# Kernel tuning notes

Hardware: AMD Instinct MI355X
Metric: run time of the kernel (lower is better)

## Reference

```python
import jax, jax.numpy as jnp
import numpy as np

NEG_SLOPE = 0.01
EPS = 1e-5


def leaky_relu(x):
    return jnp.where(x >= 0, x, NEG_SLOPE * x)


def graph_conv(x, W, src, dst, edge_weight, num_nodes):
    # DGL GraphConv, norm='both', bias=False: D_out^{-1/2} A_w D_in^{-1/2} X W
    ones = jnp.ones_like(edge_weight)
    deg_out = jnp.maximum(jax.ops.segment_sum(ones, src, num_segments=num_nodes), 1.0)
    deg_in = jnp.maximum(jax.ops.segment_sum(ones, dst, num_segments=num_nodes), 1.0)
    h = x @ W
    h = h * jax.lax.rsqrt(deg_out)[:, None]
    agg = jax.ops.segment_sum(h[src] * edge_weight[:, None], dst, num_segments=num_nodes)
    return agg * jax.lax.rsqrt(deg_in)[:, None]


def graph_norm(x, alpha, gamma, beta, batch_size):
    # GraphNorm: per-graph, per-channel mean/var; graphs are equal-sized -> reshape
    n = x.shape[0] // batch_size
    xg = x.reshape(batch_size, n, x.shape[1])
    mean = xg.mean(axis=1, keepdims=True)
    sub = xg - alpha * mean
    var = (sub * sub).mean(axis=1, keepdims=True)
    out = gamma * sub * jax.lax.rsqrt(var + EPS) + beta
    return out.reshape(x.shape)


def instance_norm(x):
    # InstanceNorm1d (affine=False) on 2D input: per-row normalization over features
    mean = x.mean(axis=-1, keepdims=True)
    var = ((x - mean) ** 2).mean(axis=-1, keepdims=True)
    return (x - mean) * jax.lax.rsqrt(var + EPS)


def setup_inputs() -> dict:
    key = jax.random.key(0)
    ks = jax.random.split(key, 9)
    B, n = 4096, 64                      # graphs, nodes per graph (equal-sized)
    N = B * n                            # 262144 nodes
    E = 8 * N                            # avg degree 8
    in_feats, conv_dim, out_conv = 64, 128, 96
    in_mlp = out_conv * n                # 6144 = in_feats_mlp
    hid = 2048
    out_feats = 256

    def kaiming(k, fin, fout):
        bound = float(np.sqrt(6.0 / ((1 + NEG_SLOPE ** 2) * fin)))
        return jax.random.uniform(k, (fin, fout), jnp.float32, -bound, bound)

    def xavier(k, fin, fout):
        bound = float(np.sqrt(6.0 / (fin + fout)))
        return jax.random.uniform(k, (fin, fout), jnp.float32, -bound, bound)

    return {
        "x": jax.random.normal(ks[0], (N, in_feats), jnp.float32),
        "edge_weight": jax.random.uniform(ks[1], (E,), jnp.float32),
        "src": jax.random.randint(ks[2], (E,), 0, N, jnp.int32),
        "dst": jax.random.randint(ks[3], (E,), 0, N, jnp.int32),
        "W1": kaiming(ks[4], in_feats, conv_dim),
        "W2": kaiming(ks[5], conv_dim, out_conv),
        "gn1_alpha": jnp.ones((conv_dim,), jnp.float32),
        "gn1_gamma": jnp.ones((conv_dim,), jnp.float32),
        "gn1_beta": jnp.zeros((conv_dim,), jnp.float32),
        "gn2_alpha": jnp.ones((out_conv,), jnp.float32),
        "gn2_gamma": jnp.ones((out_conv,), jnp.float32),
        "gn2_beta": jnp.zeros((out_conv,), jnp.float32),
        "Win": xavier(ks[6], in_mlp, hid),
        "Whid": xavier(ks[7], hid, hid // 4),
        "Wcls": xavier(ks[8], hid // 4, out_feats),
        "batch_size": B,
    }


def reference(x, edge_weight, src, dst, W1, W2, gn1_alpha, gn1_gamma, gn1_beta,
              gn2_alpha, gn2_gamma, gn2_beta, Win, Whid, Wcls, batch_size):
    N = x.shape[0]
    h = graph_conv(x, W1, src, dst, edge_weight, N)
    h = leaky_relu(h)
    h = graph_norm(h, gn1_alpha, gn1_gamma, gn1_beta, batch_size)
    h = graph_conv(h, W2, src, dst, edge_weight, N)
    h = leaky_relu(h)
    h = graph_norm(h, gn2_alpha, gn2_gamma, gn2_beta, batch_size)
    # unbatch: each equal-size graph flattened to one row [B, n*out_conv]
    h = h.reshape(batch_size, -1)
    h = instance_norm(leaky_relu(h @ Win))   # dropout is identity (p=0 / eval)
    h = instance_norm(leaky_relu(h @ Whid))
    return h @ Wcls
```

## Files before the change

### kernel.cpp

```cpp
#include <hip/hip_runtime.h>
#include <hip/hip_bf16.h>

#define NN 262144
#define EE 2097152
#define BB 4096
constexpr int INMLP = 6144;
constexpr int HID = 2048;
constexpr int HID4 = 512;
constexpr int OUTF = 256;
constexpr int NSL = 64;
constexpr int ESL = EE / NSL;
constexpr int RNODES = 32768;

typedef short s16x8 __attribute__((ext_vector_type(8)));
typedef short s16x4 __attribute__((ext_vector_type(4)));
typedef float f32x4 __attribute__((ext_vector_type(4)));

__device__ __forceinline__ float lrelu(float v) { return v >= 0.f ? v : 0.01f * v; }
__device__ __forceinline__ float bf2f(short s) {
    unsigned int u = ((unsigned int)(unsigned short)s) << 16;
    return __builtin_bit_cast(float, u);
}
__device__ __forceinline__ short f2bf(float f) {
    unsigned int u = __builtin_bit_cast(unsigned int, f);
    u = (u + 0x7fff + ((u >> 16) & 1)) >> 16;
    return (short)u;
}
__device__ __forceinline__ void async16(const void* g, void* l) {
    __builtin_amdgcn_global_load_lds((__attribute__((address_space(1))) void*)g,
                                     (__attribute__((address_space(3))) void*)l, 16, 0, 0);
}

__global__ __launch_bounds__(256) void hist_count(const int* __restrict__ dst, const int* __restrict__ src,
                                                  unsigned* __restrict__ part_din, unsigned* __restrict__ part_dout,
                                                  unsigned short* __restrict__ rankpack16) {
    __shared__ unsigned hist[RNODES / 2];
    const int S = blockIdx.x & 63;
    const int R = (blockIdx.x >> 6) & 7;
    const int T = blockIdx.x >> 9;
    for (int i = threadIdx.x; i < RNODES / 2; i += 256) hist[i] = 0;
    __syncthreads();
    const int* idxarr = T ? src : dst;
    const int4* v4 = (const int4*)(idxarr + S * ESL);
#pragma unroll 4
    for (int i = 0; i < ESL / 4 / 256; i++) {
        const int q0 = i * 256 + threadIdx.x;
        int4 q = v4[q0];
        const int ebase = S * ESL + q0 * 4;
#pragma unroll
        for (int k = 0; k < 4; k++) {
            int idx = k == 0 ? q.x : k == 1 ? q.y : k == 2 ? q.z : q.w;
            if ((idx >> 15) == R) {
                int local = idx & (RNODES - 1);
                unsigned old = atomicAdd(&hist[local >> 1], 1u << ((local & 1) * 16));
                if (T == 0) {
                    unsigned rank = (old >> ((local & 1) * 16)) & 0xffffu;
                    rankpack16[ebase + k] = (unsigned short)((S << 10) | rank);
                }
            }
        }
    }
    __syncthreads();
    unsigned* dp = (T ? part_dout : part_din) + (size_t)S * (NN / 2) + R * (RNODES / 2);
    for (int i = threadIdx.x; i < RNODES / 2; i += 256) dp[i] = hist[i];
}

__global__ __launch_bounds__(256) void deg_reduce(const unsigned* __restrict__ part_din,
                                                  const unsigned* __restrict__ part_dout,
                                                  unsigned* __restrict__ repbase_w,
                                                  float* __restrict__ ro, float* __restrict__ ri,
                                                  int* __restrict__ din) {
    int i = blockIdx.x * 256 + threadIdx.x;
    unsigned runl = 0, runh = 0, dl = 0, dh = 0;
#pragma unroll 8
    for (int S = 0; S < NSL; S++) {
        repbase_w[(size_t)S * (NN / 2) + i] = (runl & 0xffffu) | (runh << 16);
        unsigned w = part_din[(size_t)S * (NN / 2) + i];
        runl += w & 0xffffu; runh += w >> 16;
        unsigned w2 = part_dout[(size_t)S * (NN / 2) + i];
        dl += w2 & 0xffffu; dh += w2 >> 16;
    }
    int n0 = 2 * i, n1 = 2 * i + 1;
    din[n0] = (int)runl; din[n1] = (int)runh;
    ro[n0] = rsqrtf((float)(dl < 1u ? 1u : dl));
    ro[n1] = rsqrtf((float)(dh < 1u ? 1u : dh));
    ri[n0] = rsqrtf((float)(runl < 1u ? 1u : runl));
    ri[n1] = rsqrtf((float)(runh < 1u ? 1u : runh));
}

__global__ __launch_bounds__(256) void scanA(const int* __restrict__ cnt, int* __restrict__ blks) {
    __shared__ int s[256];
    int t = threadIdx.x;
    int i0 = blockIdx.x * 1024 + t * 4;
    int ts = cnt[i0] + cnt[i0 + 1] + cnt[i0 + 2] + cnt[i0 + 3];
    s[t] = ts; __syncthreads();
    for (int d = 128; d > 0; d >>= 1) { if (t < d) s[t] += s[t + d]; __syncthreads(); }
    if (t == 0) blks[blockIdx.x] = s[0];
}

__global__ __launch_bounds__(256) void scanB(int* __restrict__ blks, int* __restrict__ offN) {
    __shared__ int s[256];
    int t = threadIdx.x;
    int v = blks[t]; s[t] = v; __syncthreads();
    for (int d = 1; d < 256; d <<= 1) {
        int x = (t >= d) ? s[t - d] : 0; __syncthreads();
        s[t] += x; __syncthreads();
    }
    blks[t] = s[t] - v;
    if (t == 255) *offN = s[255];
}

__global__ __launch_bounds__(256) void scanC(const int* __restrict__ cnt, const int* __restrict__ blkoff,
                                             int* __restrict__ off) {
    __shared__ int s[256];
    int t = threadIdx.x;
    int i0 = blockIdx.x * 1024 + t * 4;
    int v0 = cnt[i0], v1 = cnt[i0 + 1], v2 = cnt[i0 + 2], v3 = cnt[i0 + 3];
    int ts = v0 + v1 + v2 + v3;
    s[t] = ts; __syncthreads();
    for (int d = 1; d < 256; d <<= 1) {
        int x = (t >= d) ? s[t - d] : 0; __syncthreads();
        s[t] += x; __syncthreads();
    }
    int base = blkoff[blockIdx.x] + (s[t] - ts);
    off[i0] = base; off[i0 + 1] = base + v0; off[i0 + 2] = base + v0 + v1; off[i0 + 3] = base + v0 + v1 + v2;
}

__global__ __launch_bounds__(256) void fill_csr(const int* __restrict__ src, const int* __restrict__ dst,
                                                const float* __restrict__ ew, const float* __restrict__ ro,
                                                const int* __restrict__ off,
                                                const unsigned short* __restrict__ repbase16,
                                                const unsigned short* __restrict__ rankpack16,
                                                int2* __restrict__ edg) {
    int e = blockIdx.x * 256 + threadIdx.x;
    int d = dst[e];
    int s = src[e];
    unsigned pk = rankpack16[e];
    int S = pk >> 10, rank = pk & 1023;
    int p = off[d] + (int)repbase16[(size_t)S * NN + d] + rank;
    edg[p] = make_int2(s, __builtin_bit_cast(int, ew[e] * ro[s]));
}

__global__ __launch_bounds__(256) void cvt_x(const float* __restrict__ X, short* __restrict__ Xb) {
    int i = (blockIdx.x * 256 + threadIdx.x) * 4;
    float4 v = *(const float4*)(X + i);
    s16x4 o = { f2bf(v.x), f2bf(v.y), f2bf(v.z), f2bf(v.w) };
    *(s16x4*)(Xb + i) = o;
}

__global__ __launch_bounds__(256) void gather64(const short* __restrict__ Xb, const int* __restrict__ offs,
                                                const int2* __restrict__ edg, short* __restrict__ Out) {
    const int lane = threadIdx.x & 63;
    const int e = lane >> 3, c = lane & 7;
    int node = blockIdx.x * 4 + (threadIdx.x >> 6);
    node = __builtin_amdgcn_readfirstlane(node);
    const int s0 = offs[node], s1 = offs[node + 1];
    float acc[8] = {};
    for (int j0 = s0; j0 < s1; j0 += 8) {
        int j = j0 + e;
        bool ok = j < s1;
        int2 pe = edg[ok ? j : s0];
        int s = pe.x;
        float w = ok ? __builtin_bit_cast(float, pe.y) : 0.f;
        s16x8 v = *(const s16x8*)&Xb[(size_t)s * 64 + c * 8];
#pragma unroll
        for (int k = 0; k < 8; k++) acc[k] = fmaf(w, bf2f(v[k]), acc[k]);
    }
#pragma unroll
    for (int off = 8; off <= 32; off <<= 1)
#pragma unroll
        for (int k = 0; k < 8; k++) acc[k] += __shfl_xor(acc[k], off);
    if (e == 0) {
        s16x8 o;
#pragma unroll
        for (int k = 0; k < 8; k++) o[k] = f2bf(acc[k]);
        *(s16x8*)&Out[(size_t)node * 64 + c * 8] = o;
    }
}

__global__ __launch_bounds__(256) void gather96(const short* __restrict__ H, const int* __restrict__ offs,
                                                const int2* __restrict__ edg, short* __restrict__ Out) {
    const int lane = threadIdx.x & 63;
    const int e = lane >> 4, c = lane & 15;
    int node = blockIdx.x * 4 + (threadIdx.x >> 6);
    node = __builtin_amdgcn_readfirstlane(node);
    const int s0 = offs[node], s1 = offs[node + 1];
    float acc[6] = {};
    for (int j0 = s0; j0 < s1; j0 += 4) {
        int j = j0 + e;
        bool ok = j < s1;
        int2 pe = edg[ok ? j : s0];
        int s = pe.x;
        float w = ok ? __builtin_bit_cast(float, pe.y) : 0.f;
        const unsigned int* hp = (const unsigned int*)(H + (size_t)s * 96 + c * 6);
        unsigned int u0 = hp[0], u1 = hp[1], u2 = hp[2];
        acc[0] = fmaf(w, bf2f((short)(u0 & 0xffff)), acc[0]);
        acc[1] = fmaf(w, bf2f((short)(u0 >> 16)), acc[1]);
        acc[2] = fmaf(w, bf2f((short)(u1 & 0xffff)), acc[2]);
        acc[3] = fmaf(w, bf2f((short)(u1 >> 16)), acc[3]);
        acc[4] = fmaf(w, bf2f((short)(u2 & 0xffff)), acc[4]);
        acc[5] = fmaf(w, bf2f((short)(u2 >> 16)), acc[5]);
    }
#pragma unroll
    for (int off = 16; off <= 32; off <<= 1)
#pragma unroll
        for (int k = 0; k < 6; k++) acc[k] += __shfl_xor(acc[k], off);
    if (e == 0) {
        unsigned int* op = (unsigned int*)(Out + (size_t)node * 96 + c * 6);
        op[0] = (unsigned short)f2bf(acc[0]) | ((unsigned)(unsigned short)f2bf(acc[1]) << 16);
        op[1] = (unsigned short)f2bf(acc[2]) | ((unsigned)(unsigned short)f2bf(acc[3]) << 16);
        op[2] = (unsigned short)f2bf(acc[4]) | ((unsigned)(unsigned short)f2bf(acc[5]) << 16);
    }
}

template <int C>
__global__ __launch_bounds__(256) void graphnorm_k(short* __restrict__ Ag, const float* __restrict__ ri,
                                                   const float* __restrict__ alpha, const float* __restrict__ gamma,
                                                   const float* __restrict__ beta) {
    __shared__ float sm[64 * C];
    __shared__ float sscale[C], sshift[C];
    const int g = blockIdx.x;
    const size_t base = (size_t)g * 64 * C;
    for (int idx = threadIdx.x; idx < 64 * C; idx += 256) {
        int i = idx / C;
        float v = bf2f(Ag[base + idx]) * ri[g * 64 + i];
        sm[idx] = lrelu(v);
    }
    __syncthreads();
    if (threadIdx.x < C) {
        int c = threadIdx.x;
        float s1 = 0.f, s2 = 0.f;
#pragma unroll 4
        for (int i = 0; i < 64; i++) { float v = sm[i * C + c]; s1 += v; s2 += v * v; }
        float m = s1 * (1.f / 64.f);
        float a = alpha[c];
        float var = s2 * (1.f / 64.f) - m * m * a * (2.f - a);
        float sc = gamma[c] * rsqrtf(var + 1e-5f);
        sscale[c] = sc;
        sshift[c] = beta[c] - sc * a * m;
    }
    __syncthreads();
    for (int idx = threadIdx.x; idx < 64 * C; idx += 256) {
        int c = idx % C;
        Ag[base + idx] = f2bf(sscale[c] * sm[idx] + sshift[c]);
    }
}

__global__ __launch_bounds__(256) void conv1_gn(const short* __restrict__ A, const short* __restrict__ BT,
                                                const float* __restrict__ ri,
                                                const float* __restrict__ alpha, const float* __restrict__ gamma,
                                                const float* __restrict__ beta, short* __restrict__ Outp) {
    __shared__ short As[128][72];
    __shared__ short Bs[128][72];
    __shared__ float sscale[2][128], sshift[2][128];
    const int t = threadIdx.x;
    const int bm = blockIdx.x * 128;
    const int wave = t >> 6, lane = t & 63;
    const int wm = (wave & 1) * 64, wn = (wave >> 1) * 64;
    const int g = wave & 1;
    const int m16 = lane & 15, quad = lane >> 4;
#pragma unroll
    for (int i = 0; i < 4; i++) {
        int idx = t + 256 * i;
        int rr = idx >> 3, kk = (idx & 7) * 8;
        *(s16x8*)&As[rr][kk] = *(const s16x8*)&A[(size_t)(bm + rr) * 64 + kk];
        *(s16x8*)&Bs[rr][kk] = *(const s16x8*)&BT[(size_t)rr * 64 + kk];
    }
    __syncthreads();
    f32x4 acc[4][4] = {};
#pragma unroll
    for (int kc = 0; kc < 2; kc++) {
        s16x8 af[4], bfr[4];
#pragma unroll
        for (int mt = 0; mt < 4; mt++) af[mt] = *(const s16x8*)&As[wm + mt * 16 + m16][kc * 32 + quad * 8];
#pragma unroll
        for (int nt = 0; nt < 4; nt++) bfr[nt] = *(const s16x8*)&Bs[wn + nt * 16 + m16][kc * 32 + quad * 8];
#pragma unroll
        for (int mt = 0; mt < 4; mt++)
#pragma unroll
            for (int nt = 0; nt < 4; nt++)
                acc[mt][nt] = __builtin_amdgcn_mfma_f32_16x16x32_bf16(af[mt], bfr[nt], acc[mt][nt], 0, 0, 0);
    }
#pragma unroll
    for (int mt = 0; mt < 4; mt++)
#pragma unroll
        for (int r4 = 0; r4 < 4; r4++) {
            float rv = ri[bm + wm + mt * 16 + quad * 4 + r4];
#pragma unroll
            for (int nt = 0; nt < 4; nt++)
                acc[mt][nt][r4] = lrelu(acc[mt][nt][r4] * rv);
        }
#pragma unroll
    for (int nt = 0; nt < 4; nt++) {
        float s1 = 0.f, s2 = 0.f;
#pragma unroll
        for (int mt = 0; mt < 4; mt++)
#pragma unroll
            for (int r4 = 0; r4 < 4; r4++) { float v = acc[mt][nt][r4]; s1 += v; s2 += v * v; }
        s1 += __shfl_xor(s1, 16); s1 += __shfl_xor(s1, 32);
        s2 += __shfl_xor(s2, 16); s2 += __shfl_xor(s2, 32);
        if (quad == 0) {
            int ch = wn + nt * 16 + m16;
            float m = s1 * (1.f / 64.f);
            float a = alpha[ch];
            float var = s2 * (1.f / 64.f) - m * m * a * (2.f - a);
            float sc = gamma[ch] * rsqrtf(var + 1e-5f);
            sscale[g][ch] = sc;
            sshift[g][ch] = beta[ch] - sc * a * m;
        }
    }
    __syncthreads();
#pragma unroll
    for (int nt = 0; nt < 4; nt++) {
        int ch = wn + nt * 16 + m16;
        float sc = sscale[g][ch], sh = sshift[g][ch];
#pragma unroll
        for (int mt = 0; mt < 4; mt++)
#pragma unroll
            for (int r4 = 0; r4 < 4; r4++) {
                int row = bm + wm + mt * 16 + quad * 4 + r4;
                Outp[(size_t)row * 128 + ch] = f2bf(sc * acc[mt][nt][r4] + sh);
            }
    }
}

__global__ __launch_bounds__(256) void conv2_mfma(const short* __restrict__ A, const short* __restrict__ BT,
                                                  short* __restrict__ H) {
    __shared__ short As[128][136];
    __shared__ short Bs[96][136];
    const int t = threadIdx.x;
    const int bm = blockIdx.x * 128;
    const int wave = t >> 6, lane = t & 63;
    const int wm = (wave & 1) * 64, wn = (wave >> 1) * 48;
    const int m16 = lane & 15, quad = lane >> 4;
#pragma unroll
    for (int i = 0; i < 8; i++) {
        int idx = t + 256 * i;
        int rr = idx >> 4, kk = (idx & 15) * 8;
        *(s16x8*)&As[rr][kk] = *(const s16x8*)&A[(size_t)(bm + rr) * 128 + kk];
    }
#pragma unroll
    for (int i = 0; i < 6; i++) {
        int idx = t + 256 * i;
        int nr = idx >> 4, kk = (idx & 15) * 8;
        *(s16x8*)&Bs[nr][kk] = *(const s16x8*)&BT[(size_t)nr * 128 + kk];
    }
    __syncthreads();
    f32x4 acc[4][3] = {};
#pragma unroll
    for (int kc = 0; kc < 4; kc++) {
        s16x8 af[4], bfr[3];
#pragma unroll
        for (int mt = 0; mt < 4; mt++) af[mt] = *(const s16x8*)&As[wm + mt * 16 + m16][kc * 32 + quad * 8];
#pragma unroll
        for (int nt = 0; nt < 3; nt++) bfr[nt] = *(const s16x8*)&Bs[wn + nt * 16 + m16][kc * 32 + quad * 8];
#pragma unroll
        for (int mt = 0; mt < 4; mt++)
#pragma unroll
            for (int nt = 0; nt < 3; nt++)
                acc[mt][nt] = __builtin_amdgcn_mfma_f32_16x16x32_bf16(af[mt], bfr[nt], acc[mt][nt], 0, 0, 0);
    }
#pragma unroll
    for (int mt = 0; mt < 4; mt++)
#pragma unroll
        for (int r4 = 0; r4 < 4; r4++) {
            int row = bm + wm + mt * 16 + quad * 4 + r4;
#pragma unroll
            for (int nt = 0; nt < 3; nt++)
                H[(size_t)row * 96 + wn + nt * 16 + m16] = f2bf(acc[mt][nt][r4]);
        }
}

__global__ __launch_bounds__(256) void transp_cvt(const float* __restrict__ W, short* __restrict__ WT,
                                                  int R, int Cc) {
    __shared__ short tile[32][33];
    const int bc = blockIdx.x * 32;
    const int br = blockIdx.y * 32;
    const int tx = threadIdx.x & 31, ty = threadIdx.x >> 5;
#pragma unroll
    for (int i = 0; i < 32; i += 8)
        tile[ty + i][tx] = f2bf(W[(size_t)(br + ty + i) * Cc + bc + tx]);
    __syncthreads();
#pragma unroll
    for (int i = 0; i < 32; i += 8)
        WT[(size_t)(bc + ty + i) * R + br + tx] = tile[tx][ty + i];
}

#define MBAR() __builtin_amdgcn_s_barrier()
#define LGKM0() asm volatile("s_waitcnt lgkmcnt(0)" ::: "memory")
#define SB0() __builtin_amdgcn_sched_barrier(0)
#define VMC4() asm volatile("s_waitcnt vmcnt(4)" ::: "memory")
#define VMC2() asm volatile("s_waitcnt vmcnt(2)" ::: "memory")
#define VMC0() asm volatile("s_waitcnt vmcnt(0)" ::: "memory")

__global__ __launch_bounds__(512, 2) void mlp1_mfma8(const short* __restrict__ A, const short* __restrict__ BT,
                                                     short* __restrict__ Cp) {
    constexpr int K = INMLP;
    __shared__ short As[2][256 * 64];
    __shared__ short Bs[2][256 * 64];
    const int t = threadIdx.x;
    const int wid = t >> 6, lane = t & 63;
    const int lrow = lane >> 3, lcol = lane & 7;
    const int scol = lcol ^ (lrow & 7);
    const int m16 = lane & 15, quad = lane >> 4, xkey = m16 & 7;
    const int wm = wid & 1, wn = wid >> 1;
    const int sw = (blockIdx.x & 7) * 32 + (blockIdx.x >> 3);
    const int bm = sw & 15, bn = (sw >> 4) & 7, z = sw >> 7;
    const short* gA = A + (size_t)(bm * 256 + lrow) * K + (size_t)z * (K / 2) + scol * 8;
    const short* gB = BT + (size_t)(bn * 256 + lrow) * K + (size_t)z * (K / 2) + scol * 8;

    f32x4 acc[8][4] = {};

#define STG(gp, Xs, s, r0, ko) \
    async16(gp + (size_t)((r0) + wid * 8) * K + (ko), &Xs[s][((r0) + wid * 8) * 64])
#define STAGE_B4(s, ko) { STG(gB, Bs, s, 0, ko); STG(gB, Bs, s, 64, ko); STG(gB, Bs, s, 128, ko); STG(gB, Bs, s, 192, ko); }
#define STAGE_A4(s, ko) { STG(gA, As, s, 0, ko); STG(gA, As, s, 128, ko); STG(gA, As, s, 64, ko); STG(gA, As, s, 192, ko); }
#define PH_LOAD(s, kc, mh) \
    { _Pragma("unroll") for (int mt = 0; mt < 4; mt++) \
          af[mt] = *(const s16x8*)&As[s][(wm * 128 + (mh) * 64 + mt * 16 + m16) * 64 + (((kc) * 4 + quad) ^ xkey) * 8]; \
      _Pragma("unroll") for (int nt = 0; nt < 4; nt++) \
          bfr[nt] = *(const s16x8*)&Bs[s][(wn * 64 + nt * 16 + m16) * 64 + (((kc) * 4 + quad) ^ xkey) * 8]; }
#define PH_MM(mh) \
    { _Pragma("unroll") for (int mt = 0; mt < 4; mt++) \
          _Pragma("unroll") for (int nt = 0; nt < 4; nt++) \
              acc[(mh) * 4 + mt][nt] = __builtin_amdgcn_mfma_f32_16x16x32_bf16(af[mt], bfr[nt], acc[(mh) * 4 + mt][nt], 0, 0, 0); }

    STAGE_B4(0, 0); STAGE_A4(0, 0);
    VMC2();
    MBAR();

    int kof = 0;
#pragma unroll 1
    for (int i = 0; i < 24; i++, kof += 128) {
        const bool st = (i < 23);
        s16x8 af[4], bfr[4];
        PH_LOAD(0, 0, 0); STAGE_B4(1, kof + 64);
        MBAR(); LGKM0(); SB0();
        __builtin_amdgcn_s_setprio(1); PH_MM(0); __builtin_amdgcn_s_setprio(0);
        VMC4(); MBAR();
        PH_LOAD(0, 0, 1); STAGE_A4(1, kof + 64);
        MBAR(); LGKM0(); SB0();
        __builtin_amdgcn_s_setprio(1); PH_MM(1); __builtin_amdgcn_s_setprio(0);
        MBAR();
        PH_LOAD(0, 1, 0);
        MBAR(); LGKM0(); SB0();
        __builtin_amdgcn_s_setprio(1); PH_MM(0); __builtin_amdgcn_s_setprio(0);
        MBAR();
        PH_LOAD(0, 1, 1);
        MBAR(); LGKM0(); SB0();
        __builtin_amdgcn_s_setprio(1); PH_MM(1); __builtin_amdgcn_s_setprio(0);
        VMC2(); MBAR();
        PH_LOAD(1, 0, 0);
        if (st) STAGE_B4(0, kof + 128);
        MBAR(); LGKM0(); SB0();
        __builtin_amdgcn_s_setprio(1); PH_MM(0); __builtin_amdgcn_s_setprio(0);
        if (st) { VMC4(); } else { VMC0(); }
        MBAR();
        PH_LOAD(1, 0, 1);
        if (st) STAGE_A4(0, kof + 128);
        MBAR(); LGKM0(); SB0();
        __builtin_amdgcn_s_setprio(1); PH_MM(1); __builtin_amdgcn_s_setprio(0);
        MBAR();
        PH_LOAD(1, 1, 0);
        MBAR(); LGKM0(); SB0();
        __builtin_amdgcn_s_setprio(1); PH_MM(0); __builtin_amdgcn_s_setprio(0);
        MBAR();
        PH_LOAD(1, 1, 1);
        MBAR(); LGKM0(); SB0();
        __builtin_amdgcn_s_setprio(1); PH_MM(1); __builtin_amdgcn_s_setprio(0);
        if (st) { VMC2(); }
        MBAR();
    }

    short* C = Cp + (size_t)z * BB * HID;
    const int r0 = bm * 256 + wm * 128 + quad * 4;
    const int c0 = bn * 256 + wn * 64 + m16;
#pragma unroll
    for (int mt = 0; mt < 8; mt++)
#pragma unroll
        for (int nt = 0; nt < 4; nt++)
#pragma unroll
            for (int r4 = 0; r4 < 4; r4++)
                C[(size_t)(r0 + mt * 16 + r4) * HID + c0 + nt * 16] = f2bf(acc[mt][nt][r4]);
#undef STG
#undef STAGE_A4
#undef STAGE_B4
#undef PH_LOAD
#undef PH_MM
}

__global__ __launch_bounds__(256) void rownorm_hid(short* __restrict__ D0, const short* __restrict__ D1) {
    const size_t base = (size_t)blockIdx.x * HID;
    float v[8];
    float s1 = 0.f, s2 = 0.f;
    const int c0 = threadIdx.x * 8;
    {
        s16x8 a = *(const s16x8*)&D0[base + c0];
        s16x8 b = *(const s16x8*)&D1[base + c0];
#pragma unroll
        for (int k = 0; k < 8; k++) {
            float x = lrelu(bf2f(a[k]) + bf2f(b[k]));
            v[k] = x; s1 += x; s2 += x * x;
        }
    }
#pragma unroll
    for (int o = 32; o > 0; o >>= 1) { s1 += __shfl_down(s1, o); s2 += __shfl_down(s2, o); }
    __shared__ float w1[4], w2[4];
    if ((threadIdx.x & 63) == 0) { w1[threadIdx.x >> 6] = s1; w2[threadIdx.x >> 6] = s2; }
    __syncthreads();
    s1 = w1[0] + w1[1] + w1[2] + w1[3];
    s2 = w2[0] + w2[1] + w2[2] + w2[3];
    float m = s1 * (1.f / HID);
    float inv = rsqrtf(s2 * (1.f / HID) - m * m + 1e-5f);
    s16x8 o;
#pragma unroll
    for (int k = 0; k < 8; k++) o[k] = f2bf((v[k] - m) * inv);
    *(s16x8*)&D0[base + c0] = o;
}

template <bool ABF16, bool LEAKY>
__global__ __launch_bounds__(256) void mfma_gemm(const float* __restrict__ Af, const short* __restrict__ Ab,
                                                 const short* __restrict__ BT,
                                                 float* __restrict__ C, int M, int Nn, int K) {
    __shared__ short As[64][40];
    __shared__ short Bs[64][40];
    const int t = threadIdx.x;
    const int bm = blockIdx.x * 64, bn = blockIdx.y * 64;
    const int wave = t >> 6, lane = t & 63;
    const int wm = (wave & 1) * 32, wn = (wave >> 1) * 32;
    const int m16 = lane & 15, quad = lane >> 4;
    const int rr = t >> 2, kk = (t & 3) * 8;
    f32x4 acc[2][2] = {};
    for (int k0 = 0; k0 < K; k0 += 32) {
        if (ABF16) {
            *(s16x8*)&As[rr][kk] = *(const s16x8*)&Ab[(size_t)(bm + rr) * K + k0 + kk];
        } else {
            const float* ap = &Af[(size_t)(bm + rr) * K + k0 + kk];
            float4 v0 = *(const float4*)ap;
            float4 v1 = *(const float4*)(ap + 4);
            s16x8 a8;
            a8[0] = f2bf(v0.x); a8[1] = f2bf(v0.y); a8[2] = f2bf(v0.z); a8[3] = f2bf(v0.w);
            a8[4] = f2bf(v1.x); a8[5] = f2bf(v1.y); a8[6] = f2bf(v1.z); a8[7] = f2bf(v1.w);
            *(s16x8*)&As[rr][kk] = a8;
        }
        *(s16x8*)&Bs[rr][kk] = *(const s16x8*)&BT[(size_t)(bn + rr) * K + k0 + kk];
        __syncthreads();
        s16x8 af[2], bfr[2];
#pragma unroll
        for (int mt = 0; mt < 2; mt++) af[mt] = *(const s16x8*)&As[wm + mt * 16 + m16][quad * 8];
#pragma unroll
        for (int nt = 0; nt < 2; nt++) bfr[nt] = *(const s16x8*)&Bs[wn + nt * 16 + m16][quad * 8];
#pragma unroll
        for (int mt = 0; mt < 2; mt++)
#pragma unroll
            for (int nt = 0; nt < 2; nt++)
                acc[mt][nt] = __builtin_amdgcn_mfma_f32_16x16x32_bf16(af[mt], bfr[nt], acc[mt][nt], 0, 0, 0);
        __syncthreads();
    }
#pragma unroll
    for (int mt = 0; mt < 2; mt++)
#pragma unroll
        for (int nt = 0; nt < 2; nt++)
#pragma unroll
            for (int r4 = 0; r4 < 4; r4++) {
                int row = bm + wm + mt * 16 + quad * 4 + r4;
                int col = bn + wn + nt * 16 + m16;
                float v = acc[mt][nt][r4];
                if (LEAKY) v = lrelu(v);
                C[(size_t)row * Nn + col] = v;
            }
}

template <int NC>
__global__ __launch_bounds__(256) void rownorm(float* __restrict__ Y) {
    float* p = Y + (size_t)blockIdx.x * NC;
    float s1 = 0.f, s2 = 0.f;
    for (int c = threadIdx.x; c < NC; c += 256) { float v = p[c]; s1 += v; s2 += v * v; }
#pragma unroll
    for (int o = 32; o > 0; o >>= 1) { s1 += __shfl_down(s1, o); s2 += __shfl_down(s2, o); }
    __shared__ float w1[4], w2[4];
    if ((threadIdx.x & 63) == 0) { w1[threadIdx.x >> 6] = s1; w2[threadIdx.x >> 6] = s2; }
    __syncthreads();
    s1 = w1[0] + w1[1] + w1[2] + w1[3];
    s2 = w2[0] + w2[1] + w2[2] + w2[3];
    float m = s1 * (1.f / NC);
    float inv = rsqrtf(s2 * (1.f / NC) - m * m + 1e-5f);
    for (int c = threadIdx.x; c < NC; c += 256) p[c] = (p[c] - m) * inv;
}

extern "C" void kernel_launch(void* const* d_in, const int* in_sizes, int n_in,
                              void* d_out, int out_size, void* d_ws, size_t ws_size,
                              hipStream_t stream) {
    const float* x    = (const float*)d_in[0];
    const float* ew   = (const float*)d_in[1];
    const int*   src  = (const int*)d_in[2];
    const int*   dst  = (const int*)d_in[3];
    const float* W1   = (const float*)d_in[4];
    const float* W2   = (const float*)d_in[5];
    const float* a1   = (const float*)d_in[6];
    const float* g1   = (const float*)d_in[7];
    const float* b1   = (const float*)d_in[8];
    const float* a2   = (const float*)d_in[9];
    const float* g2   = (const float*)d_in[10];
    const float* b2   = (const float*)d_in[11];
    const float* Win  = (const float*)d_in[12];
    const float* Whid = (const float*)d_in[13];
    const float* Wcls = (const float*)d_in[14];
    float* out = (float*)d_out;

    float* ro   = (float*)d_ws;
    float* ri   = ro + NN;
    int*   din  = (int*)(ri + NN);
    int*   offs = din + NN;
    int*   blks = offs + NN + 4;
    short* w1t  = (short*)(blks + 256);
    short* w2t  = w1t + 128 * 64;
    int2*  edg  = (int2*)(((size_t)(w2t + 96 * 128) + 15) & ~(size_t)15);
    short* Abf  = (short*)(edg + EE);
    short* Bbf  = Abf + (size_t)NN * 128;
    short* xbf  = Abf;
    short* aggx = Abf + (size_t)NN * 64;
    unsigned*       part_din   = (unsigned*)Abf;
    unsigned*       part_dout  = part_din + (size_t)NSL * (NN / 2);
    unsigned*       repbase_w  = (unsigned*)Bbf;
    unsigned short* rankpack16 = (unsigned short*)(repbase_w + (size_t)NSL * (NN / 2));
    short* WinT = Abf;
    short* D0   = (short*)((char*)Abf + 25165824);
    short* D1   = D0 + (size_t)BB * HID;
    float* Y2   = (float*)edg;
    short* WhidT = Bbf;
    short* WclsT = WhidT + (size_t)HID4 * HID;

    hist_count<<<2 * 8 * NSL, 256, 0, stream>>>(dst, src, part_din, part_dout, rankpack16);
    deg_reduce<<<NN / 512, 256, 0, stream>>>(part_din, part_dout, repbase_w, ro, ri, din);

    scanA<<<NN / 1024, 256, 0, stream>>>(din, blks);
    scanB<<<1, 256, 0, stream>>>(blks, offs + NN);
    scanC<<<NN / 1024, 256, 0, stream>>>(din, blks, offs);
    fill_csr<<<EE / 256, 256, 0, stream>>>(src, dst, ew, ro, offs,
                                           (const unsigned short*)repbase_w, rankpack16, edg);

    cvt_x<<<NN * 64 / 1024, 256, 0, stream>>>(x, xbf);
    transp_cvt<<<dim3(128 / 32, 64 / 32), 256, 0, stream>>>(W1, w1t, 64, 128);
    gather64<<<NN / 4, 256, 0, stream>>>(xbf, offs, edg, aggx);
    conv1_gn<<<NN / 128, 256, 0, stream>>>(aggx, w1t, ri, a1, g1, b1, Bbf);

    transp_cvt<<<dim3(96 / 32, 128 / 32), 256, 0, stream>>>(W2, w2t, 128, 96);
    conv2_mfma<<<NN / 128, 256, 0, stream>>>(Bbf, w2t, Abf);
    gather96<<<NN / 4, 256, 0, stream>>>(Abf, offs, edg, Bbf);
    graphnorm_k<96><<<BB, 256, 0, stream>>>(Bbf, ri, a2, g2, b2);

    transp_cvt<<<dim3(HID / 32, INMLP / 32), 256, 0, stream>>>(Win, WinT, INMLP, HID);
    mlp1_mfma8<<<256, 512, 0, stream>>>(Bbf, WinT, D0);
    transp_cvt<<<dim3(HID4 / 32, HID / 32), 256, 0, stream>>>(Whid, WhidT, HID, HID4);
    transp_cvt<<<dim3(OUTF / 32, HID4 / 32), 256, 0, stream>>>(Wcls, WclsT, HID4, OUTF);
    rownorm_hid<<<BB, 256, 0, stream>>>(D0, D1);
    mfma_gemm<true, true><<<dim3(BB / 64, HID4 / 64), 256, 0, stream>>>(nullptr, D0, WhidT, Y2, BB, HID4, HID);
    rownorm<HID4><<<BB, 256, 0, stream>>>(Y2);
    mfma_gemm<false, false><<<dim3(BB / 64, OUTF / 64), 256, 0, stream>>>(Y2, nullptr, WclsT, out, BB, OUTF, HID4);
}
```

Baseline: 797.3 us.

## Restructure MLP1 GEMM main loop with register double-buffered fragments and partial waits

Rewrites the K-loop of the large bf16 MFMA GEMM so that LDS fragment loads for the next sub-phase are issued into alternate register buffers while the current MFMAs run. Partial lgkmcnt waits replace the full drains before each MFMA group. Both shared-memory stages are prefetched up front, and per-tile barriers drop from about eight to two. The aim is to hide LDS latency and cut barrier stalls, at the cost of higher register pressure under the 512x2 launch bounds and a more delicate wait-count schedule.

After: 824.1 us. +3.4%, slower.

```diff
diff --git a/kernel.cpp b/kernel.cpp
--- a/kernel.cpp
+++ b/kernel.cpp
@@ -387,11 +387,9 @@
 }
 
 #define MBAR() __builtin_amdgcn_s_barrier()
-#define LGKM0() asm volatile("s_waitcnt lgkmcnt(0)" ::: "memory")
 #define SB0() __builtin_amdgcn_sched_barrier(0)
-#define VMC4() asm volatile("s_waitcnt vmcnt(4)" ::: "memory")
-#define VMC2() asm volatile("s_waitcnt vmcnt(2)" ::: "memory")
-#define VMC0() asm volatile("s_waitcnt vmcnt(0)" ::: "memory")
+#define LGKM(n) asm volatile("s_waitcnt lgkmcnt(" #n ")" ::: "memory")
+#define VMC(n) asm volatile("s_waitcnt vmcnt(" #n ")" ::: "memory")
 
 __global__ __launch_bounds__(512, 2) void mlp1_mfma8(const short* __restrict__ A, const short* __restrict__ BT,
                                                      short* __restrict__ Cp) {
@@ -409,67 +407,55 @@
     const short* gA = A + (size_t)(bm * 256 + lrow) * K + (size_t)z * (K / 2) + scol * 8;
     const short* gB = BT + (size_t)(bn * 256 + lrow) * K + (size_t)z * (K / 2) + scol * 8;
 
+    s16x8 afA[4], afB[4], b0[4], b1[4];
     f32x4 acc[8][4] = {};
 
-#define STG(gp, Xs, s, r0, ko) \
-    async16(gp + (size_t)((r0) + wid * 8) * K + (ko), &Xs[s][((r0) + wid * 8) * 64])
-#define STAGE_B4(s, ko) { STG(gB, Bs, s, 0, ko); STG(gB, Bs, s, 64, ko); STG(gB, Bs, s, 128, ko); STG(gB, Bs, s, 192, ko); }
-#define STAGE_A4(s, ko) { STG(gA, As, s, 0, ko); STG(gA, As, s, 128, ko); STG(gA, As, s, 64, ko); STG(gA, As, s, 192, ko); }
-#define PH_LOAD(s, kc, mh) \
+#define STG(gp, Xs, S, r0, ko) \
+    async16(gp + (size_t)((r0) + wid * 8) * K + (ko), &Xs[S][((r0) + wid * 8) * 64])
+#define STAGE_B4(S, ko) { STG(gB, Bs, S, 0, ko); STG(gB, Bs, S, 64, ko); STG(gB, Bs, S, 128, ko); STG(gB, Bs, S, 192, ko); }
+#define STAGE_A4(S, ko) { STG(gA, As, S, 0, ko); STG(gA, As, S, 64, ko); STG(gA, As, S, 128, ko); STG(gA, As, S, 192, ko); }
+#define LD_AF(S, kc, mh, d) \
     { _Pragma("unroll") for (int mt = 0; mt < 4; mt++) \
-          af[mt] = *(const s16x8*)&As[s][(wm * 128 + (mh) * 64 + mt * 16 + m16) * 64 + (((kc) * 4 + quad) ^ xkey) * 8]; \
-      _Pragma("unroll") for (int nt = 0; nt < 4; nt++) \
-          bfr[nt] = *(const s16x8*)&Bs[s][(wn * 64 + nt * 16 + m16) * 64 + (((kc) * 4 + quad) ^ xkey) * 8]; }
-#define PH_MM(mh) \
+          d[mt] = *(const s16x8*)&As[S][(wm * 128 + (mh) * 64 + mt * 16 + m16) * 64 + (((kc) * 4 + quad) ^ xkey) * 8]; }
+#define LD_BF(S, kc, d) \
+    { _Pragma("unroll") for (int nt = 0; nt < 4; nt++) \
+          d[nt] = *(const s16x8*)&Bs[S][(wn * 64 + nt * 16 + m16) * 64 + (((kc) * 4 + quad) ^ xkey) * 8]; }
+#define MM(mh, a, b) \
     { _Pragma("unroll") for (int mt = 0; mt < 4; mt++) \
           _Pragma("unroll") for (int nt = 0; nt < 4; nt++) \
-              acc[(mh) * 4 + mt][nt] = __builtin_amdgcn_mfma_f32_16x16x32_bf16(af[mt], bfr[nt], acc[(mh) * 4 + mt][nt], 0, 0, 0); }
+              acc[(mh) * 4 + mt][nt] = __builtin_amdgcn_mfma_f32_16x16x32_bf16(a[mt], b[nt], acc[(mh) * 4 + mt][nt], 0, 0, 0); }
 
     STAGE_B4(0, 0); STAGE_A4(0, 0);
-    VMC2();
-    MBAR();
-
-    int kof = 0;
+    STAGE_B4(1, 64); STAGE_A4(1, 64);
+    VMC(8);
+    MBAR(); SB0();
+    LD_AF(0, 0, 0, afA); LD_BF(0, 0, b0);
+
+#define TILE(S, S2, j) { \
+         \
+        LD_AF(S, 0, 1, afB); \
+        LGKM(4); SB0(); \
+        __builtin_amdgcn_s_setprio(1); MM(0, afA, b0); __builtin_amdgcn_s_setprio(0); \
+         \
+        LD_AF(S, 1, 0, afA); LD_BF(S, 1, b1); \
+        LGKM(8); SB0(); \
+        __builtin_amdgcn_s_setprio(1); MM(1, afB, b0); __builtin_amdgcn_s_setprio(0); \
+         \
+        LD_AF(S, 1, 1, afB); \
+        LGKM(4); VMC(0); SB0(); MBAR(); SB0(); \
+        __builtin_amdgcn_s_setprio(1); MM(0, afA, b1); __builtin_amdgcn_s_setprio(0); \
+         \
+        if ((j) <= 46) { LD_AF(S2, 0, 0, afA); LD_BF(S2, 0, b0); LGKM(8); } \
+        else { LGKM(0); } \
+        SB0(); MBAR(); SB0(); \
+        if ((j) <= 45) { STAGE_B4(S, ((j) + 2) * 64); STAGE_A4(S, ((j) + 2) * 64); } \
+        __builtin_amdgcn_s_setprio(1); MM(1, afB, b1); __builtin_amdgcn_s_setprio(0); \
+    }
+
 #pragma unroll 1
-    for (int i = 0; i < 24; i++, kof += 128) {
-        const bool st = (i < 23);
-        s16x8 af[4], bfr[4];
-        PH_LOAD(0, 0, 0); STAGE_B4(1, kof + 64);
-        MBAR(); LGKM0(); SB0();
-        __builtin_amdgcn_s_setprio(1); PH_MM(0); __builtin_amdgcn_s_setprio(0);
-        VMC4(); MBAR();
-        PH_LOAD(0, 0, 1); STAGE_A4(1, kof + 64);
-        MBAR(); LGKM0(); SB0();
-        __builtin_amdgcn_s_setprio(1); PH_MM(1); __builtin_amdgcn_s_setprio(0);
-        MBAR();
-        PH_LOAD(0, 1, 0);
-        MBAR(); LGKM0(); SB0();
-        __builtin_amdgcn_s_setprio(1); PH_MM(0); __builtin_amdgcn_s_setprio(0);
-        MBAR();
-        PH_LOAD(0, 1, 1);
-        MBAR(); LGKM0(); SB0();
-        __builtin_amdgcn_s_setprio(1); PH_MM(1); __builtin_amdgcn_s_setprio(0);
-        VMC2(); MBAR();
-        PH_LOAD(1, 0, 0);
-        if (st) STAGE_B4(0, kof + 128);
-        MBAR(); LGKM0(); SB0();
-        __builtin_amdgcn_s_setprio(1); PH_MM(0); __builtin_amdgcn_s_setprio(0);
-        if (st) { VMC4(); } else { VMC0(); }
-        MBAR();
-        PH_LOAD(1, 0, 1);
-        if (st) STAGE_A4(0, kof + 128);
-        MBAR(); LGKM0(); SB0();
-        __builtin_amdgcn_s_setprio(1); PH_MM(1); __builtin_amdgcn_s_setprio(0);
-        MBAR();
-        PH_LOAD(1, 1, 0);
-        MBAR(); LGKM0(); SB0();
-        __builtin_amdgcn_s_setprio(1); PH_MM(0); __builtin_amdgcn_s_setprio(0);
-        MBAR();
-        PH_LOAD(1, 1, 1);
-        MBAR(); LGKM0(); SB0();
-        __builtin_amdgcn_s_setprio(1); PH_MM(1); __builtin_amdgcn_s_setprio(0);
-        if (st) { VMC2(); }
-        MBAR();
+    for (int p = 0; p < 24; ++p) {
+        TILE(0, 1, 2 * p);
+        TILE(1, 0, 2 * p + 1);
     }
 
     short* C = Cp + (size_t)z * BB * HID;
@@ -485,8 +471,10 @@
 #undef STG
 #undef STAGE_A4
 #undef STAGE_B4
-#undef PH_LOAD
-#undef PH_MM
+#undef LD_AF
+#undef LD_BF
+#undef MM
+#undef TILE
 }
 
 __global__ __launch_bounds__(256) void rownorm_hid(short* __restrict__ D0, const short* __restrict__ D1) {
```

## Replace sliced LDS histogram CSR build with global atomic degree and rank

Applied to the files above, without the earlier changes.

Swaps the partitioned shared-memory histogram (64 edge slices by 8 node ranges, then a per-slice prefix reduction) for a simple global-atomic pass that counts in/out degree and records each edge's rank within its destination. The CSR fill then uses the offset plus rank directly, removing the large partial-count buffers and the replicated-base lookup. This trades many redundant index scans and big intermediate writes for 4M global atomics, which may contend and serialize on hot nodes. Edge order within each CSR row becomes nondeterministic, so float accumulation order can vary between runs.

After: 900.5 us. 1.13x slower.

```diff
diff --git a/kernel.cpp b/kernel.cpp
--- a/kernel.cpp
+++ b/kernel.cpp
@@ -8,9 +8,6 @@
 constexpr int HID = 2048;
 constexpr int HID4 = 512;
 constexpr int OUTF = 256;
-constexpr int NSL = 64;
-constexpr int ESL = EE / NSL;
-constexpr int RNODES = 32768;
 
 typedef short s16x8 __attribute__((ext_vector_type(8)));
 typedef short s16x4 __attribute__((ext_vector_type(4)));
@@ -31,61 +28,28 @@
                                      (__attribute__((address_space(3))) void*)l, 16, 0, 0);
 }
 
-__global__ __launch_bounds__(256) void hist_count(const int* __restrict__ dst, const int* __restrict__ src,
-                                                  unsigned* __restrict__ part_din, unsigned* __restrict__ part_dout,
-                                                  unsigned short* __restrict__ rankpack16) {
-    __shared__ unsigned hist[RNODES / 2];
-    const int S = blockIdx.x & 63;
-    const int R = (blockIdx.x >> 6) & 7;
-    const int T = blockIdx.x >> 9;
-    for (int i = threadIdx.x; i < RNODES / 2; i += 256) hist[i] = 0;
-    __syncthreads();
-    const int* idxarr = T ? src : dst;
-    const int4* v4 = (const int4*)(idxarr + S * ESL);
-#pragma unroll 4
-    for (int i = 0; i < ESL / 4 / 256; i++) {
-        const int q0 = i * 256 + threadIdx.x;
-        int4 q = v4[q0];
-        const int ebase = S * ESL + q0 * 4;
-#pragma unroll
-        for (int k = 0; k < 4; k++) {
-            int idx = k == 0 ? q.x : k == 1 ? q.y : k == 2 ? q.z : q.w;
-            if ((idx >> 15) == R) {
-                int local = idx & (RNODES - 1);
-                unsigned old = atomicAdd(&hist[local >> 1], 1u << ((local & 1) * 16));
-                if (T == 0) {
-                    unsigned rank = (old >> ((local & 1) * 16)) & 0xffffu;
-                    rankpack16[ebase + k] = (unsigned short)((S << 10) | rank);
-                }
-            }
-        }
-    }
-    __syncthreads();
-    unsigned* dp = (T ? part_dout : part_din) + (size_t)S * (NN / 2) + R * (RNODES / 2);
-    for (int i = threadIdx.x; i < RNODES / 2; i += 256) dp[i] = hist[i];
-}
-
-__global__ __launch_bounds__(256) void deg_reduce(const unsigned* __restrict__ part_din,
-                                                  const unsigned* __restrict__ part_dout,
-                                                  unsigned* __restrict__ repbase_w,
-                                                  float* __restrict__ ro, float* __restrict__ ri,
-                                                  int* __restrict__ din) {
+__global__ __launch_bounds__(256) void zero2(int* __restrict__ a, int* __restrict__ b) {
+    int i = (blockIdx.x * 256 + threadIdx.x) * 4;
+    *(int4*)(a + i) = make_int4(0, 0, 0, 0);
+    *(int4*)(b + i) = make_int4(0, 0, 0, 0);
+}
+
+__global__ __launch_bounds__(256) void deg_rank(const int* __restrict__ src, const int* __restrict__ dst,
+                                                int* __restrict__ din, int* __restrict__ dout,
+                                                unsigned* __restrict__ rank) {
+    int e = blockIdx.x * 256 + threadIdx.x;
+    int d = dst[e];
+    int s = src[e];
+    rank[e] = (unsigned)atomicAdd(&din[d], 1);
+    atomicAdd(&dout[s], 1);
+}
+
+__global__ __launch_bounds__(256) void rsq_deg(const int* __restrict__ din, const int* __restrict__ dout,
+                                               float* __restrict__ ri, float* __restrict__ ro) {
     int i = blockIdx.x * 256 + threadIdx.x;
-    unsigned runl = 0, runh = 0, dl = 0, dh = 0;
-#pragma unroll 8
-    for (int S = 0; S < NSL; S++) {
-        repbase_w[(size_t)S * (NN / 2) + i] = (runl & 0xffffu) | (runh << 16);
-        unsigned w = part_din[(size_t)S * (NN / 2) + i];
-        runl += w & 0xffffu; runh += w >> 16;
-        unsigned w2 = part_dout[(size_t)S * (NN / 2) + i];
-        dl += w2 & 0xffffu; dh += w2 >> 16;
-    }
-    int n0 = 2 * i, n1 = 2 * i + 1;
-    din[n0] = (int)runl; din[n1] = (int)runh;
-    ro[n0] = rsqrtf((float)(dl < 1u ? 1u : dl));
-    ro[n1] = rsqrtf((float)(dh < 1u ? 1u : dh));
-    ri[n0] = rsqrtf((float)(runl < 1u ? 1u : runl));
-    ri[n1] = rsqrtf((float)(runh < 1u ? 1u : runh));
+    int a = din[i], b = dout[i];
+    ri[i] = rsqrtf((float)(a < 1 ? 1 : a));
+    ro[i] = rsqrtf((float)(b < 1 ? 1 : b));
 }
 
 __global__ __launch_bounds__(256) void scanA(const int* __restrict__ cnt, int* __restrict__ blks) {
@@ -126,18 +90,14 @@
     off[i0] = base; off[i0 + 1] = base + v0; off[i0 + 2] = base + v0 + v1; off[i0 + 3] = base + v0 + v1 + v2;
 }
 
-__global__ __launch_bounds__(256) void fill_csr(const int* __restrict__ src, const int* __restrict__ dst,
-                                                const float* __restrict__ ew, const float* __restrict__ ro,
-                                                const int* __restrict__ off,
-                                                const unsigned short* __restrict__ repbase16,
-                                                const unsigned short* __restrict__ rankpack16,
-                                                int2* __restrict__ edg) {
+__global__ __launch_bounds__(256) void fill_csr2(const int* __restrict__ src, const int* __restrict__ dst,
+                                                 const float* __restrict__ ew, const float* __restrict__ ro,
+                                                 const int* __restrict__ off, const unsigned* __restrict__ rank,
+                                                 int2* __restrict__ edg) {
     int e = blockIdx.x * 256 + threadIdx.x;
     int d = dst[e];
     int s = src[e];
-    unsigned pk = rankpack16[e];
-    int S = pk >> 10, rank = pk & 1023;
-    int p = off[d] + (int)repbase16[(size_t)S * NN + d] + rank;
+    int p = off[d] + (int)rank[e];
     edg[p] = make_int2(s, __builtin_bit_cast(int, ew[e] * ro[s]));
 }
 
@@ -620,10 +580,8 @@
     short* Bbf  = Abf + (size_t)NN * 128;
     short* xbf  = Abf;
     short* aggx = Abf + (size_t)NN * 64;
-    unsigned*       part_din   = (unsigned*)Abf;
-    unsigned*       part_dout  = part_din + (size_t)NSL * (NN / 2);
-    unsigned*       repbase_w  = (unsigned*)Bbf;
-    unsigned short* rankpack16 = (unsigned short*)(repbase_w + (size_t)NSL * (NN / 2));
+    int*      dout = (int*)Abf;
+    unsigned* rank = (unsigned*)Bbf;
     short* WinT = Abf;
     short* D0   = (short*)((char*)Abf + 25165824);
     short* D1   = D0 + (size_t)BB * HID;
@@ -631,14 +589,14 @@
     short* WhidT = Bbf;
     short* WclsT = WhidT + (size_t)HID4 * HID;
 
-    hist_count<<<2 * 8 * NSL, 256, 0, stream>>>(dst, src, part_din, part_dout, rankpack16);
-    deg_reduce<<<NN / 512, 256, 0, stream>>>(part_din, part_dout, repbase_w, ro, ri, din);
+    zero2<<<NN / 1024, 256, 0, stream>>>(din, dout);
+    deg_rank<<<EE / 256, 256, 0, stream>>>(src, dst, din, dout, rank);
+    rsq_deg<<<NN / 256, 256, 0, stream>>>(din, dout, ri, ro);
 
     scanA<<<NN / 1024, 256, 0, stream>>>(din, blks);
     scanB<<<1, 256, 0, stream>>>(blks, offs + NN);
     scanC<<<NN / 1024, 256, 0, stream>>>(din, blks, offs);
-    fill_csr<<<EE / 256, 256, 0, stream>>>(src, dst, ew, ro, offs,
-                                           (const unsigned short*)repbase_w, rankpack16, edg);
+    fill_csr2<<<EE / 256, 256, 0, stream>>>(src, dst, ew, ro, offs, rank, edg);
 
     cvt_x<<<NN * 64 / 1024, 256, 0, stream>>>(x, xbf);
     transp_cvt<<<dim3(128 / 32, 64 / 32), 256, 0, stream>>>(W1, w1t, 64, 128);
```

## Fuse edge gathers into conv1 GEMM and graph-norm kernels

Applied to the files above, without the earlier changes.

The first-layer neighbour aggregation now runs inside the conv1 GEMM block, writing aggregated rows straight into shared memory instead of a global intermediate. The second-layer gather is fused with graph norm, one block per graph. This removes two kernel launches and the global write and re-read of the aggregated features. In exchange, gather parallelism drops: each wave now handles 16-32 nodes in sequence instead of one, and there are far fewer blocks (2048 or 4096 instead of 65536), which may reduce the memory-latency hiding available to the irregular gathers.

Result: slower. 907.9 us (+13.9%).

```diff
diff --git a/kernel.cpp b/kernel.cpp
--- a/kernel.cpp
+++ b/kernel.cpp
@@ -148,108 +148,11 @@
     *(s16x4*)(Xb + i) = o;
 }
 
-__global__ __launch_bounds__(256) void gather64(const short* __restrict__ Xb, const int* __restrict__ offs,
-                                                const int2* __restrict__ edg, short* __restrict__ Out) {
-    const int lane = threadIdx.x & 63;
-    const int e = lane >> 3, c = lane & 7;
-    int node = blockIdx.x * 4 + (threadIdx.x >> 6);
-    node = __builtin_amdgcn_readfirstlane(node);
-    const int s0 = offs[node], s1 = offs[node + 1];
-    float acc[8] = {};
-    for (int j0 = s0; j0 < s1; j0 += 8) {
-        int j = j0 + e;
-        bool ok = j < s1;
-        int2 pe = edg[ok ? j : s0];
-        int s = pe.x;
-        float w = ok ? __builtin_bit_cast(float, pe.y) : 0.f;
-        s16x8 v = *(const s16x8*)&Xb[(size_t)s * 64 + c * 8];
-#pragma unroll
-        for (int k = 0; k < 8; k++) acc[k] = fmaf(w, bf2f(v[k]), acc[k]);
-    }
-#pragma unroll
-    for (int off = 8; off <= 32; off <<= 1)
-#pragma unroll
-        for (int k = 0; k < 8; k++) acc[k] += __shfl_xor(acc[k], off);
-    if (e == 0) {
-        s16x8 o;
-#pragma unroll
-        for (int k = 0; k < 8; k++) o[k] = f2bf(acc[k]);
-        *(s16x8*)&Out[(size_t)node * 64 + c * 8] = o;
-    }
-}
-
-__global__ __launch_bounds__(256) void gather96(const short* __restrict__ H, const int* __restrict__ offs,
-                                                const int2* __restrict__ edg, short* __restrict__ Out) {
-    const int lane = threadIdx.x & 63;
-    const int e = lane >> 4, c = lane & 15;
-    int node = blockIdx.x * 4 + (threadIdx.x >> 6);
-    node = __builtin_amdgcn_readfirstlane(node);
-    const int s0 = offs[node], s1 = offs[node + 1];
-    float acc[6] = {};
-    for (int j0 = s0; j0 < s1; j0 += 4) {
-        int j = j0 + e;
-        bool ok = j < s1;
-        int2 pe = edg[ok ? j : s0];
-        int s = pe.x;
-        float w = ok ? __builtin_bit_cast(float, pe.y) : 0.f;
-        const unsigned int* hp = (const unsigned int*)(H + (size_t)s * 96 + c * 6);
-        unsigned int u0 = hp[0], u1 = hp[1], u2 = hp[2];
-        acc[0] = fmaf(w, bf2f((short)(u0 & 0xffff)), acc[0]);
-        acc[1] = fmaf(w, bf2f((short)(u0 >> 16)), acc[1]);
-        acc[2] = fmaf(w, bf2f((short)(u1 & 0xffff)), acc[2]);
-        acc[3] = fmaf(w, bf2f((short)(u1 >> 16)), acc[3]);
-        acc[4] = fmaf(w, bf2f((short)(u2 & 0xffff)), acc[4]);
-        acc[5] = fmaf(w, bf2f((short)(u2 >> 16)), acc[5]);
-    }
-#pragma unroll
-    for (int off = 16; off <= 32; off <<= 1)
-#pragma unroll
-        for (int k = 0; k < 6; k++) acc[k] += __shfl_xor(acc[k], off);
-    if (e == 0) {
-        unsigned int* op = (unsigned int*)(Out + (size_t)node * 96 + c * 6);
-        op[0] = (unsigned short)f2bf(acc[0]) | ((unsigned)(unsigned short)f2bf(acc[1]) << 16);
-        op[1] = (unsigned short)f2bf(acc[2]) | ((unsigned)(unsigned short)f2bf(acc[3]) << 16);
-        op[2] = (unsigned short)f2bf(acc[4]) | ((unsigned)(unsigned short)f2bf(acc[5]) << 16);
-    }
-}
-
-template <int C>
-__global__ __launch_bounds__(256) void graphnorm_k(short* __restrict__ Ag, const float* __restrict__ ri,
-                                                   const float* __restrict__ alpha, const float* __restrict__ gamma,
-                                                   const float* __restrict__ beta) {
-    __shared__ float sm[64 * C];
-    __shared__ float sscale[C], sshift[C];
-    const int g = blockIdx.x;
-    const size_t base = (size_t)g * 64 * C;
-    for (int idx = threadIdx.x; idx < 64 * C; idx += 256) {
-        int i = idx / C;
-        float v = bf2f(Ag[base + idx]) * ri[g * 64 + i];
-        sm[idx] = lrelu(v);
-    }
-    __syncthreads();
-    if (threadIdx.x < C) {
-        int c = threadIdx.x;
-        float s1 = 0.f, s2 = 0.f;
-#pragma unroll 4
-        for (int i = 0; i < 64; i++) { float v = sm[i * C + c]; s1 += v; s2 += v * v; }
-        float m = s1 * (1.f / 64.f);
-        float a = alpha[c];
-        float var = s2 * (1.f / 64.f) - m * m * a * (2.f - a);
-        float sc = gamma[c] * rsqrtf(var + 1e-5f);
-        sscale[c] = sc;
-        sshift[c] = beta[c] - sc * a * m;
-    }
-    __syncthreads();
-    for (int idx = threadIdx.x; idx < 64 * C; idx += 256) {
-        int c = idx % C;
-        Ag[base + idx] = f2bf(sscale[c] * sm[idx] + sshift[c]);
-    }
-}
-
-__global__ __launch_bounds__(256) void conv1_gn(const short* __restrict__ A, const short* __restrict__ BT,
-                                                const float* __restrict__ ri,
-                                                const float* __restrict__ alpha, const float* __restrict__ gamma,
-                                                const float* __restrict__ beta, short* __restrict__ Outp) {
+__global__ __launch_bounds__(256) void conv1_gather_gn(const short* __restrict__ Xb, const int* __restrict__ offs,
+                                                       const int2* __restrict__ edg, const short* __restrict__ BT,
+                                                       const float* __restrict__ ri,
+                                                       const float* __restrict__ alpha, const float* __restrict__ gamma,
+                                                       const float* __restrict__ beta, short* __restrict__ Outp) {
     __shared__ short As[128][72];
     __shared__ short Bs[128][72];
     __shared__ float sscale[2][128], sshift[2][128];
@@ -263,8 +166,36 @@
     for (int i = 0; i < 4; i++) {
         int idx = t + 256 * i;
         int rr = idx >> 3, kk = (idx & 7) * 8;
-        *(s16x8*)&As[rr][kk] = *(const s16x8*)&A[(size_t)(bm + rr) * 64 + kk];
         *(s16x8*)&Bs[rr][kk] = *(const s16x8*)&BT[(size_t)rr * 64 + kk];
+    }
+    {
+        const int e = lane >> 3, c = lane & 7;
+        for (int i = 0; i < 32; i++) {
+            const int row = wave * 32 + i;
+            const int node = bm + row;
+            const int s0 = offs[node], s1 = offs[node + 1];
+            float acc[8] = {};
+            for (int j0 = s0; j0 < s1; j0 += 8) {
+                int j = j0 + e;
+                bool ok = j < s1;
+                int2 pe = edg[ok ? j : s0];
+                int s = pe.x;
+                float w = ok ? __builtin_bit_cast(float, pe.y) : 0.f;
+                s16x8 v = *(const s16x8*)&Xb[(size_t)s * 64 + c * 8];
+#pragma unroll
+                for (int k = 0; k < 8; k++) acc[k] = fmaf(w, bf2f(v[k]), acc[k]);
+            }
+#pragma unroll
+            for (int off = 8; off <= 32; off <<= 1)
+#pragma unroll
+                for (int k = 0; k < 8; k++) acc[k] += __shfl_xor(acc[k], off);
+            if (e == 0) {
+                s16x8 o;
+#pragma unroll
+                for (int k = 0; k < 8; k++) o[k] = f2bf(acc[k]);
+                *(s16x8*)&As[row][c * 8] = o;
+            }
+        }
     }
     __syncthreads();
     f32x4 acc[4][4] = {};
@@ -369,6 +300,68 @@
             for (int nt = 0; nt < 3; nt++)
                 H[(size_t)row * 96 + wn + nt * 16 + m16] = f2bf(acc[mt][nt][r4]);
         }
+}
+
+__global__ __launch_bounds__(256) void gather96_gn(const short* __restrict__ H, const int* __restrict__ offs,
+                                                   const int2* __restrict__ edg, const float* __restrict__ ri,
+                                                   const float* __restrict__ alpha, const float* __restrict__ gamma,
+                                                   const float* __restrict__ beta, short* __restrict__ Out) {
+    __shared__ float sm[64 * 96];
+    __shared__ float sscale[96], sshift[96];
+    const int g = blockIdx.x;
+    const int t = threadIdx.x;
+    const int wave = t >> 6, lane = t & 63;
+    const int e = lane >> 4, c = lane & 15;
+    for (int i = 0; i < 16; i++) {
+        const int row = wave * 16 + i;
+        const int node = g * 64 + row;
+        const int s0 = offs[node], s1 = offs[node + 1];
+        float acc[6] = {};
+        for (int j0 = s0; j0 < s1; j0 += 4) {
+            int j = j0 + e;
+            bool ok = j < s1;
+            int2 pe = edg[ok ? j : s0];
+            int s = pe.x;
+            float w = ok ? __builtin_bit_cast(float, pe.y) : 0.f;
+            const unsigned int* hp = (const unsigned int*)(H + (size_t)s * 96 + c * 6);
+            unsigned int u0 = hp[0], u1 = hp[1], u2 = hp[2];
+            acc[0] = fmaf(w, bf2f((short)(u0 & 0xffff)), acc[0]);
+            acc[1] = fmaf(w, bf2f((short)(u0 >> 16)), acc[1]);
+            acc[2] = fmaf(w, bf2f((short)(u1 & 0xffff)), acc[2]);
+            acc[3] = fmaf(w, bf2f((short)(u1 >> 16)), acc[3]);
+            acc[4] = fmaf(w, bf2f((short)(u2 & 0xffff)), acc[4]);
+            acc[5] = fmaf(w, bf2f((short)(u2 >> 16)), acc[5]);
+        }
+#pragma unroll
+        for (int off = 16; off <= 32; off <<= 1)
+#pragma unroll
+            for (int k = 0; k < 6; k++) acc[k] += __shfl_xor(acc[k], off);
+        if (e == 0) {
+            float rv = ri[node];
+#pragma unroll
+            for (int k = 0; k < 6; k++)
+                sm[row * 96 + c * 6 + k] = lrelu(bf2f(f2bf(acc[k])) * rv);
+        }
+    }
+    __syncthreads();
+    if (t < 96) {
+        int c2 = t;
+        float s1 = 0.f, s2 = 0.f;
+#pragma unroll 4
+        for (int i = 0; i < 64; i++) { float v = sm[i * 96 + c2]; s1 += v; s2 += v * v; }
+        float m = s1 * (1.f / 64.f);
+        float a = alpha[c2];
+        float var = s2 * (1.f / 64.f) - m * m * a * (2.f - a);
+        float sc = gamma[c2] * rsqrtf(var + 1e-5f);
+        sscale[c2] = sc;
+        sshift[c2] = beta[c2] - sc * a * m;
+    }
+    __syncthreads();
+    const size_t base = (size_t)g * 64 * 96;
+    for (int idx = t; idx < 64 * 96; idx += 256) {
+        int c2 = idx % 96;
+        Out[base + idx] = f2bf(sscale[c2] * sm[idx] + sshift[c2]);
+    }
 }
 
 __global__ __launch_bounds__(256) void transp_cvt(const float* __restrict__ W, short* __restrict__ WT,
@@ -619,7 +612,6 @@
     short* Abf  = (short*)(edg + EE);
     short* Bbf  = Abf + (size_t)NN * 128;
     short* xbf  = Abf;
-    short* aggx = Abf + (size_t)NN * 64;
     unsigned*       part_din   = (unsigned*)Abf;
     unsigned*       part_dout  = part_din + (size_t)NSL * (NN / 2);
     unsigned*       repbase_w  = (unsigned*)Bbf;
@@ -642,13 +634,11 @@
 
     cvt_x<<<NN * 64 / 1024, 256, 0, stream>>>(x, xbf);
     transp_cvt<<<dim3(128 / 32, 64 / 32), 256, 0, stream>>>(W1, w1t, 64, 128);
-    gather64<<<NN / 4, 256, 0, stream>>>(xbf, offs, edg, aggx);
-    conv1_gn<<<NN / 128, 256, 0, stream>>>(aggx, w1t, ri, a1, g1, b1, Bbf);
+    conv1_gather_gn<<<NN / 128, 256, 0, stream>>>(xbf, offs, edg, w1t, ri, a1, g1, b1, Bbf);
 
     transp_cvt<<<dim3(96 / 32, 128 / 32), 256, 0, stream>>>(W2, w2t, 128, 96);
     conv2_mfma<<<NN / 128, 256, 0, stream>>>(Bbf, w2t, Abf);
-    gather96<<<NN / 4, 256, 0, stream>>>(Abf, offs, edg, Bbf);
-    graphnorm_k<96><<<BB, 256, 0, stream>>>(Bbf, ri, a2, g2, b2);
+    gather96_gn<<<BB, 256, 0, stream>>>(Abf, offs, edg, ri, a2, g2, b2, Bbf);
 
     transp_cvt<<<dim3(HID / 32, INMLP / 32), 256, 0, stream>>>(Win, WinT, INMLP, HID);
     mlp1_mfma8<<<256, 512, 0, stream>>>(Bbf, WinT, D0);
```
